# Optimization experiments

Hardware: AMD Instinct MI355X
Metric: run time of the kernel (lower is better)

## Reference

```python
import jax, jax.numpy as jnp
import numpy as np

B, N, D, H = 4, 2048, 512, 8
HD = D // H
SCALE = D ** (-0.5)  # module uses embed_dim**-0.5, not head_dim**-0.5


def setup_inputs() -> dict:
    key = jax.random.key(0)
    k1, k2, k3, k4 = jax.random.split(key, 4)
    x = jax.random.normal(k1, (B, N, D), dtype=jnp.float32)
    # qkv: Linear(D, 3D, bias=False); store as [D, 3D] (x @ W_qkv)
    w_qkv = jax.random.normal(k2, (D, 3 * D), dtype=jnp.float32) * (D ** -0.5)
    # out_proj: Linear(D, D) with bias
    w_out = jax.random.normal(k3, (D, D), dtype=jnp.float32) * (D ** -0.5)
    b_out = jax.random.normal(k4, (D,), dtype=jnp.float32) * 0.01
    return {"x": x, "w_qkv": w_qkv, "w_out": w_out, "b_out": b_out}


def reference(x, w_qkv, w_out, b_out):
    # qkv projection -> [B, N, 3, H, HD] -> split
    qkv = (x @ w_qkv).reshape(B, N, 3, H, HD)
    q = qkv[:, :, 0].transpose(0, 2, 1, 3)  # [B, H, N, HD]
    k = qkv[:, :, 1].transpose(0, 2, 1, 3)
    v = qkv[:, :, 2].transpose(0, 2, 1, 3)
    attn = jnp.einsum("bhqd,bhkd->bhqk", q, k) * SCALE  # [B, H, N, N]
    attn = jax.nn.softmax(attn, axis=-1)
    out = jnp.einsum("bhqk,bhkd->bhqd", attn, v)  # [B, H, N, HD]
    out = out.transpose(0, 2, 1, 3).reshape(B, N, D)
    return out @ w_out + b_out
```

## Files before the change

### kernel.cpp

```cpp
#include <hip/hip_runtime.h>

typedef __attribute__((ext_vector_type(4))) float f32x4;
typedef __attribute__((ext_vector_type(16))) float f32x16;
typedef __attribute__((ext_vector_type(8))) short short8;

#define DEV static __device__ __forceinline__

DEV unsigned short f2bf(float f) {
  union { float f; unsigned u; } x; x.f = f;
  unsigned r = x.u + 0x7fffu + ((x.u >> 16) & 1u);
  return (unsigned short)(r >> 16);
}

DEV float bf2f(unsigned short u) {
  union { unsigned u; float f; } x; x.u = ((unsigned)u) << 16;
  return x.f;
}

DEV f32x4 mfma16(short8 a, short8 b, f32x4 c) {
  return __builtin_amdgcn_mfma_f32_16x16x32_bf16(a, b, c, 0, 0, 0);
}

DEV f32x16 mfma32(short8 a, short8 b, f32x16 c) {
  return __builtin_amdgcn_mfma_f32_32x32x16_bf16(a, b, c, 0, 0, 0);
}

DEV void gload16(const void* g, void* l) {
  __builtin_amdgcn_global_load_lds(
      (const __attribute__((address_space(1))) void*)g,
      (__attribute__((address_space(3))) void*)l, 16, 0, 0);
}

DEV float exp2f_fast(float x) {
  float r;
  asm("v_exp_f32 %0, %1" : "=v"(r) : "v"(x));
  return r;
}

DEV unsigned cvtpk(float lo, float hi) {
  unsigned r;
  asm("v_cvt_pk_bf16_f32 %0, %1, %2" : "=v"(r) : "v"(lo), "v"(hi));
  return r;
}

DEV short8 mk8(unsigned w0, unsigned w1, unsigned w2, unsigned w3) {
  union { unsigned u[4]; short8 s; } x;
  x.u[0] = w0; x.u[1] = w1; x.u[2] = w2; x.u[3] = w3;
  return x.s;
}

__global__ __launch_bounds__(256) void k_convert(const float* __restrict__ in,
                                                 unsigned short* __restrict__ out) {
  size_t i = (size_t)blockIdx.x * 256 + threadIdx.x;
  const f32x4* p = (const f32x4*)(in + i * 8);
  f32x4 a = p[0], b = p[1];
  short8 r;
  r[0] = f2bf(a[0]); r[1] = f2bf(a[1]); r[2] = f2bf(a[2]); r[3] = f2bf(a[3]);
  r[4] = f2bf(b[0]); r[5] = f2bf(b[1]); r[6] = f2bf(b[2]); r[7] = f2bf(b[3]);
  *(short8*)(out + i * 8) = r;
}

__global__ __launch_bounds__(256) void k_transpose_f32_bf16(
    const float* __restrict__ in, unsigned short* __restrict__ out, int R, int C) {
  __shared__ unsigned short T[64 * 72];
  int r0 = blockIdx.y * 64, c0 = blockIdx.x * 64;
  int t = threadIdx.x;
  int rr = t >> 2, seg = t & 3;
  const float* p = in + (size_t)(r0 + rr) * C + c0 + seg * 16;
#pragma unroll
  for (int q = 0; q < 4; ++q) {
    f32x4 v = *(const f32x4*)(p + q * 4);
#pragma unroll
    for (int e = 0; e < 4; ++e) T[rr * 72 + seg * 16 + q * 4 + e] = f2bf(v[e]);
  }
  __syncthreads();
  short8 o0, o1;
#pragma unroll
  for (int e = 0; e < 8; ++e) o0[e] = (short)T[(seg * 16 + e) * 72 + rr];
#pragma unroll
  for (int e = 0; e < 8; ++e) o1[e] = (short)T[(seg * 16 + 8 + e) * 72 + rr];
  unsigned short* q2 = out + (size_t)(c0 + rr) * R + r0 + seg * 16;
  *(short8*)q2 = o0;
  *(short8*)(q2 + 8) = o1;
}

__global__ __launch_bounds__(256) void k_build_vt(const unsigned short* __restrict__ qkv,
                                                  unsigned short* __restrict__ vt) {
  __shared__ unsigned short T[64 * 72];
  int n0 = blockIdx.x * 64;
  int bh = blockIdx.y;
  int b = bh >> 3, h = bh & 7;
  int t = threadIdx.x;
  int rr = t >> 2, seg = t & 3;
  const unsigned short* p =
      qkv + (size_t)(b * 2048 + n0 + rr) * 1536 + 1024 + h * 64 + seg * 16;
  *(short8*)&T[rr * 72 + seg * 16] = *(const short8*)p;
  *(short8*)&T[rr * 72 + seg * 16 + 8] = *(const short8*)(p + 8);
  __syncthreads();
  short8 o0, o1;
#pragma unroll
  for (int e = 0; e < 8; ++e) o0[e] = (short)T[(seg * 16 + e) * 72 + rr];
#pragma unroll
  for (int e = 0; e < 8; ++e) o1[e] = (short)T[(seg * 16 + 8 + e) * 72 + rr];
  unsigned short* q2 = vt + (size_t)(bh * 64 + rr) * 2048 + n0 + seg * 16;
  *(short8*)q2 = o0;
  *(short8*)(q2 + 8) = o1;
}

template <bool F32OUT>
__global__ __launch_bounds__(256) void k_gemm_bt(
    const unsigned short* __restrict__ A, const unsigned short* __restrict__ Bt,
    void* __restrict__ Cp, const float* __restrict__ bias, int M, int N, int K) {
  __shared__ unsigned short Asm[128 * 64];
  __shared__ unsigned short Bsm[128 * 64];
  const int tid = threadIdx.x;
  const int lane = tid & 63, w = tid >> 6;
  const int wr = w >> 1, wc = w & 1;
  const int bm = blockIdx.y * 128, bn = blockIdx.x * 128;
  const int l15 = lane & 15, l4 = lane >> 4;
  f32x4 acc[4][4] = {};
  for (int k0 = 0; k0 < K; k0 += 64) {
    __syncthreads();
#pragma unroll
    for (int j = 0; j < 4; ++j) {
      int c = j * 256 + tid;
      gload16(A + (size_t)(bm + (c >> 3)) * K + k0 + ((c & 7) << 3),
              Asm + (size_t)(j * 256 + w * 64) * 8);
    }
#pragma unroll
    for (int j = 0; j < 4; ++j) {
      int c = j * 256 + tid;
      gload16(Bt + (size_t)(bn + (c >> 3)) * K + k0 + ((c & 7) << 3),
              Bsm + (size_t)(j * 256 + w * 64) * 8);
    }
    __syncthreads();
#pragma unroll
    for (int kc = 0; kc < 2; ++kc) {
      short8 av[4], bv[4];
#pragma unroll
      for (int i = 0; i < 4; ++i)
        av[i] = *(const short8*)&Asm[(wr * 64 + i * 16 + l15) * 64 + kc * 32 + l4 * 8];
#pragma unroll
      for (int j = 0; j < 4; ++j)
        bv[j] = *(const short8*)&Bsm[(wc * 64 + j * 16 + l15) * 64 + kc * 32 + l4 * 8];
#pragma unroll
      for (int i = 0; i < 4; ++i)
#pragma unroll
        for (int j = 0; j < 4; ++j)
          acc[i][j] = mfma16(av[i], bv[j], acc[i][j]);
    }
  }
#pragma unroll
  for (int i = 0; i < 4; ++i) {
#pragma unroll
    for (int j = 0; j < 4; ++j) {
      int col = bn + wc * 64 + j * 16 + l15;
      float bb = 0.f;
      if constexpr (F32OUT) bb = bias[col];
#pragma unroll
      for (int v = 0; v < 4; ++v) {
        int row = bm + wr * 64 + i * 16 + l4 * 4 + v;
        if constexpr (F32OUT) {
          ((float*)Cp)[(size_t)row * N + col] = acc[i][j][v] + bb;
        } else {
          ((unsigned short*)Cp)[(size_t)row * N + col] = f2bf(acc[i][j][v]);
        }
      }
    }
  }
}

__global__ __launch_bounds__(256, 2) void k_attn2(const unsigned short* __restrict__ qkv,
                                                  const unsigned short* __restrict__ vtg,
                                                  unsigned short* __restrict__ O) {
  __shared__ unsigned short Ksm[2][64 * 64];
  __shared__ unsigned short Vsm[2][64 * 64];
  __shared__ float sml[4][32];
  const int tid = threadIdx.x;
  const int lane = tid & 63, w = tid >> 6;
  const int l31 = lane & 31, hi = lane >> 5;
  const int bh = blockIdx.y, b = bh >> 3, h = bh & 7;
  const int q0 = blockIdx.x * 128 + w * 32;
  const float CL = 0.044194173824159216f * 1.4426950408889634f;

  short8 qf[4];
  {
    const unsigned short* qp = qkv + (size_t)(b * 2048 + q0 + l31) * 1536 + h * 64;
#pragma unroll
    for (int ks = 0; ks < 4; ++ks) {
      short8 raw = *(const short8*)(qp + ks * 16 + hi * 8);
      short8 f;
#pragma unroll
      for (int e = 0; e < 8; ++e)
        f[e] = (short)f2bf(bf2f((unsigned short)raw[e]) * CL);
      qf[ks] = f;
    }
  }

  const int sr = tid >> 3, seg = tid & 7;
  const unsigned short* kg = qkv + (size_t)b * 2048 * 1536 + 512 + h * 64 + seg * 8;
  const unsigned short* vg = vtg + (size_t)bh * 64 * 2048 + seg * 8;
  const int wr1 = sr + 32;
  const int so0 = sr * 64 + ((seg * 8) ^ ((sr & 7) << 3));
  const int so1 = wr1 * 64 + ((seg * 8) ^ ((wr1 & 7) << 3));

  {
    short8 a = *(const short8*)(kg + (size_t)sr * 1536);
    short8 c = *(const short8*)(kg + (size_t)wr1 * 1536);
    short8 d0 = *(const short8*)(vg + (size_t)sr * 2048);
    short8 d1 = *(const short8*)(vg + (size_t)wr1 * 2048);
    *(short8*)&Ksm[0][so0] = a;  *(short8*)&Ksm[0][so1] = c;
    *(short8*)&Vsm[0][so0] = d0; *(short8*)&Vsm[0][so1] = d1;
  }
  __syncthreads();

  f32x16 oacc0 = {}, oacc1 = {};
  float m_run = 0.f, l_run = 0.f;
  const int rsw = (l31 & 7) << 3;

  for (int t = 0; t < 32; ++t) {
    const int cur = t & 1;
    const unsigned short* kb = Ksm[cur];
    const unsigned short* vb = Vsm[cur];

    short8 pk0, pk1, pv0, pv1;
    if (t < 31) {
      int kv = (t + 1) * 64;
      pk0 = *(const short8*)(kg + (size_t)(kv + sr) * 1536);
      pk1 = *(const short8*)(kg + (size_t)(kv + wr1) * 1536);
      pv0 = *(const short8*)(vg + (size_t)sr * 2048 + kv);
      pv1 = *(const short8*)(vg + (size_t)wr1 * 2048 + kv);
    }

    f32x16 st[2] = {};
#pragma unroll
    for (int ks = 0; ks < 4; ++ks) {
      int col = ks * 16 + hi * 8;
      short8 kf0 = *(const short8*)&kb[l31 * 64 + (col ^ rsw)];
      short8 kf1 = *(const short8*)&kb[(32 + l31) * 64 + (col ^ rsw)];
      st[0] = mfma32(kf0, qf[ks], st[0]);
      st[1] = mfma32(kf1, qf[ks], st[1]);
    }

    float tm[8];
#pragma unroll
    for (int r = 0; r < 8; ++r)
      tm[r] = fmaxf(fmaxf(st[0][r], st[0][r + 8]), fmaxf(st[1][r], st[1][r + 8]));
    float pm = fmaxf(fmaxf(fmaxf(tm[0], tm[1]), fmaxf(tm[2], tm[3])),
                     fmaxf(fmaxf(tm[4], tm[5]), fmaxf(tm[6], tm[7])));
    pm = fmaxf(pm, __shfl_xor(pm, 32));

    if (!__all(pm <= m_run + 11.5f)) {
      float mn = fmaxf(m_run, pm);
      float al = exp2f_fast(m_run - mn);
      sml[w][l31] = al;
#pragma unroll
      for (int r = 0; r < 16; ++r) {
        float a = sml[w][(r & 3) + 8 * (r >> 2) + 4 * hi];
        oacc0[r] *= a;
        oacc1[r] *= a;
      }
      l_run *= al;
      m_run = mn;
    }

    float lsum = 0.f;
    short8 pa[4];
#pragma unroll
    for (int s = 0; s < 2; ++s) {
      float p[16];
      float la = 0.f, lb = 0.f;
#pragma unroll
      for (int r = 0; r < 8; ++r) { p[r] = exp2f_fast(st[s][r] - m_run); la += p[r]; }
#pragma unroll
      for (int r = 8; r < 16; ++r) { p[r] = exp2f_fast(st[s][r] - m_run); lb += p[r]; }
      lsum += la + lb;
#pragma unroll
      for (int g = 0; g < 2; ++g) {
        unsigned pkA0 = cvtpk(p[8 * g + 0], p[8 * g + 1]);
        unsigned pkA1 = cvtpk(p[8 * g + 2], p[8 * g + 3]);
        unsigned pkB0 = cvtpk(p[8 * g + 4], p[8 * g + 5]);
        unsigned pkB1 = cvtpk(p[8 * g + 6], p[8 * g + 7]);
        unsigned tA0 = __shfl_xor(pkA0, 32), tA1 = __shfl_xor(pkA1, 32);
        unsigned tB0 = __shfl_xor(pkB0, 32), tB1 = __shfl_xor(pkB1, 32);
        unsigned w0 = hi ? tB0 : pkA0;
        unsigned w1 = hi ? tB1 : pkA1;
        unsigned w2 = hi ? pkB0 : tA0;
        unsigned w3 = hi ? pkB1 : tA1;
        pa[2 * s + g] = mk8(w0, w1, w2, w3);
      }
    }
    lsum += __shfl_xor(lsum, 32);
    l_run += lsum;

#pragma unroll
    for (int ks = 0; ks < 4; ++ks) {
      int col = ks * 16 + hi * 8;
      short8 vf0 = *(const short8*)&vb[l31 * 64 + (col ^ rsw)];
      short8 vf1 = *(const short8*)&vb[(32 + l31) * 64 + (col ^ rsw)];
      oacc0 = mfma32(pa[ks], vf0, oacc0);
      oacc1 = mfma32(pa[ks], vf1, oacc1);
    }

    if (t < 31) {
      unsigned short* kn = Ksm[cur ^ 1];
      unsigned short* vn = Vsm[cur ^ 1];
      *(short8*)&kn[so0] = pk0; *(short8*)&kn[so1] = pk1;
      *(short8*)&vn[so0] = pv0; *(short8*)&vn[so1] = pv1;
    }
    __syncthreads();
  }

  sml[w][l31] = l_run;
#pragma unroll
  for (int r = 0; r < 16; ++r) {
    int qd = (r & 3) + 8 * (r >> 2) + 4 * hi;
    float linv = 1.0f / sml[w][qd];
    size_t row = (size_t)(b * 2048 + q0 + qd) * 512 + h * 64;
    O[row + l31] = f2bf(oacc0[r] * linv);
    O[row + 32 + l31] = f2bf(oacc1[r] * linv);
  }
}

extern "C" void kernel_launch(void* const* d_in, const int* in_sizes, int n_in,
                              void* d_out, int out_size, void* d_ws, size_t ws_size,
                              hipStream_t stream) {
  const float* x = (const float*)d_in[0];
  const float* w_qkv = (const float*)d_in[1];
  const float* w_out = (const float*)d_in[2];
  const float* b_out = (const float*)d_in[3];
  float* out = (float*)d_out;
  char* ws = (char*)d_ws;

  unsigned short* xb    = (unsigned short*)(ws + 0);
  unsigned short* wqkvT = (unsigned short*)(ws + 8388608);
  unsigned short* woutT = (unsigned short*)(ws + 9961472);
  unsigned short* qkvb  = (unsigned short*)(ws + 10485760);
  unsigned short* vtb   = (unsigned short*)(ws + 35651584);
  unsigned short* Ob    = (unsigned short*)(ws + 44040192);

  k_convert<<<2048, 256, 0, stream>>>(x, xb);
  k_transpose_f32_bf16<<<dim3(24, 8), 256, 0, stream>>>(w_qkv, wqkvT, 512, 1536);
  k_transpose_f32_bf16<<<dim3(8, 8), 256, 0, stream>>>(w_out, woutT, 512, 512);
  k_gemm_bt<false><<<dim3(12, 64), 256, 0, stream>>>(xb, wqkvT, (void*)qkvb, nullptr,
                                                     8192, 1536, 512);
  k_build_vt<<<dim3(32, 32), 256, 0, stream>>>(qkvb, vtb);
  k_attn2<<<dim3(16, 32), 256, 0, stream>>>(qkvb, vtb, Ob);
  k_gemm_bt<true><<<dim3(4, 64), 256, 0, stream>>>(Ob, woutT, (void*)out, b_out,
                                                   8192, 512, 512);
}
```

Before: 183.5 us.

## Software-pipeline QK^T one tile ahead with triple-buffered V in attention

The attention kernel now computes the QK^T scores for tile t+1 while doing softmax and PV on tile t. Global prefetch moves to two tiles ahead, with K double-buffered and V triple-buffered in LDS. MFMA sections are wrapped in s_setprio so they get issue priority. The per-row rescale and normalise broadcasts now use lane shuffles instead of a shared-memory array. The cost is more registers (an extra pair of score accumulators) and more LDS, which may hurt occupancy at two blocks per CU.

New measurement: 184.7 us. About the same (+0.7%).

```diff
diff --git a/kernel.cpp b/kernel.cpp
--- a/kernel.cpp
+++ b/kernel.cpp
@@ -170,12 +170,11 @@
   }
 }
 
-__global__ __launch_bounds__(256, 2) void k_attn2(const unsigned short* __restrict__ qkv,
+__global__ __launch_bounds__(256, 2) void k_attn3(const unsigned short* __restrict__ qkv,
                                                   const unsigned short* __restrict__ vtg,
                                                   unsigned short* __restrict__ O) {
-  __shared__ unsigned short Ksm[2][64 * 64];
-  __shared__ unsigned short Vsm[2][64 * 64];
-  __shared__ float sml[4][32];
+  __shared__ unsigned short Ks[2][4096];
+  __shared__ unsigned short Vs[3][4096];
   const int tid = threadIdx.x;
   const int lane = tid & 63, w = tid >> 6;
   const int l31 = lane & 31, hi = lane >> 5;
@@ -200,52 +199,81 @@
   const int sr = tid >> 3, seg = tid & 7;
   const unsigned short* kg = qkv + (size_t)b * 2048 * 1536 + 512 + h * 64 + seg * 8;
   const unsigned short* vg = vtg + (size_t)bh * 64 * 2048 + seg * 8;
-  const int wr1 = sr + 32;
   const int so0 = sr * 64 + ((seg * 8) ^ ((sr & 7) << 3));
-  const int so1 = wr1 * 64 + ((seg * 8) ^ ((wr1 & 7) << 3));
+  const int so1 = so0 + 32 * 64;
 
   {
-    short8 a = *(const short8*)(kg + (size_t)sr * 1536);
-    short8 c = *(const short8*)(kg + (size_t)wr1 * 1536);
-    short8 d0 = *(const short8*)(vg + (size_t)sr * 2048);
-    short8 d1 = *(const short8*)(vg + (size_t)wr1 * 2048);
-    *(short8*)&Ksm[0][so0] = a;  *(short8*)&Ksm[0][so1] = c;
-    *(short8*)&Vsm[0][so0] = d0; *(short8*)&Vsm[0][so1] = d1;
+    short8 k0a = *(const short8*)(kg + (size_t)sr * 1536);
+    short8 k0b = *(const short8*)(kg + (size_t)(sr + 32) * 1536);
+    short8 v0a = *(const short8*)(vg + (size_t)sr * 2048);
+    short8 v0b = *(const short8*)(vg + (size_t)(sr + 32) * 2048);
+    short8 k1a = *(const short8*)(kg + (size_t)(64 + sr) * 1536);
+    short8 k1b = *(const short8*)(kg + (size_t)(64 + sr + 32) * 1536);
+    short8 v1a = *(const short8*)(vg + (size_t)sr * 2048 + 64);
+    short8 v1b = *(const short8*)(vg + (size_t)(sr + 32) * 2048 + 64);
+    *(short8*)&Ks[0][so0] = k0a; *(short8*)&Ks[0][so1] = k0b;
+    *(short8*)&Vs[0][so0] = v0a; *(short8*)&Vs[0][so1] = v0b;
+    *(short8*)&Ks[1][so0] = k1a; *(short8*)&Ks[1][so1] = k1b;
+    *(short8*)&Vs[1][so0] = v1a; *(short8*)&Vs[1][so1] = v1b;
   }
   __syncthreads();
 
-  f32x16 oacc0 = {}, oacc1 = {};
-  float m_run = 0.f, l_run = 0.f;
   const int rsw = (l31 & 7) << 3;
 
-  for (int t = 0; t < 32; ++t) {
-    const int cur = t & 1;
-    const unsigned short* kb = Ksm[cur];
-    const unsigned short* vb = Vsm[cur];
-
-    short8 pk0, pk1, pv0, pv1;
-    if (t < 31) {
-      int kv = (t + 1) * 64;
-      pk0 = *(const short8*)(kg + (size_t)(kv + sr) * 1536);
-      pk1 = *(const short8*)(kg + (size_t)(kv + wr1) * 1536);
-      pv0 = *(const short8*)(vg + (size_t)sr * 2048 + kv);
-      pv1 = *(const short8*)(vg + (size_t)wr1 * 2048 + kv);
-    }
-
-    f32x16 st[2] = {};
+  f32x16 st0 = {}, st1 = {};
+  {
+    const unsigned short* kb = Ks[0];
+    __builtin_amdgcn_s_setprio(1);
 #pragma unroll
     for (int ks = 0; ks < 4; ++ks) {
       int col = ks * 16 + hi * 8;
       short8 kf0 = *(const short8*)&kb[l31 * 64 + (col ^ rsw)];
       short8 kf1 = *(const short8*)&kb[(32 + l31) * 64 + (col ^ rsw)];
-      st[0] = mfma32(kf0, qf[ks], st[0]);
-      st[1] = mfma32(kf1, qf[ks], st[1]);
+      st0 = mfma32(kf0, qf[ks], st0);
+      st1 = mfma32(kf1, qf[ks], st1);
+    }
+    __builtin_amdgcn_s_setprio(0);
+  }
+  __syncthreads();
+
+  unsigned short* kread = Ks[1];
+  unsigned short* kwrite = Ks[0];
+  unsigned short* vcur = Vs[0];
+  unsigned short* vnxt = Vs[1];
+  unsigned short* vstg = Vs[2];
+
+  f32x16 oacc0 = {}, oacc1 = {};
+  float m_run = 0.f, l_run = 0.f;
+
+  for (int t = 0; t < 32; ++t) {
+    short8 pk0, pk1, pv0, pv1;
+    const bool has2 = (t < 30);
+    if (has2) {
+      int kv = (t + 2) * 64;
+      pk0 = *(const short8*)(kg + (size_t)(kv + sr) * 1536);
+      pk1 = *(const short8*)(kg + (size_t)(kv + sr + 32) * 1536);
+      pv0 = *(const short8*)(vg + (size_t)sr * 2048 + kv);
+      pv1 = *(const short8*)(vg + (size_t)(sr + 32) * 2048 + kv);
+    }
+
+    f32x16 ns0 = {}, ns1 = {};
+    if (t < 31) {
+      __builtin_amdgcn_s_setprio(1);
+#pragma unroll
+      for (int ks = 0; ks < 4; ++ks) {
+        int col = ks * 16 + hi * 8;
+        short8 kf0 = *(const short8*)&kread[l31 * 64 + (col ^ rsw)];
+        short8 kf1 = *(const short8*)&kread[(32 + l31) * 64 + (col ^ rsw)];
+        ns0 = mfma32(kf0, qf[ks], ns0);
+        ns1 = mfma32(kf1, qf[ks], ns1);
+      }
+      __builtin_amdgcn_s_setprio(0);
     }
 
     float tm[8];
 #pragma unroll
     for (int r = 0; r < 8; ++r)
-      tm[r] = fmaxf(fmaxf(st[0][r], st[0][r + 8]), fmaxf(st[1][r], st[1][r + 8]));
+      tm[r] = fmaxf(fmaxf(st0[r], st0[r + 8]), fmaxf(st1[r], st1[r + 8]));
     float pm = fmaxf(fmaxf(fmaxf(tm[0], tm[1]), fmaxf(tm[2], tm[3])),
                      fmaxf(fmaxf(tm[4], tm[5]), fmaxf(tm[6], tm[7])));
     pm = fmaxf(pm, __shfl_xor(pm, 32));
@@ -253,10 +281,10 @@
     if (!__all(pm <= m_run + 11.5f)) {
       float mn = fmaxf(m_run, pm);
       float al = exp2f_fast(m_run - mn);
-      sml[w][l31] = al;
 #pragma unroll
       for (int r = 0; r < 16; ++r) {
-        float a = sml[w][(r & 3) + 8 * (r >> 2) + 4 * hi];
+        int qd = (r & 3) + 8 * (r >> 2) + 4 * hi;
+        float a = __shfl(al, qd);
         oacc0[r] *= a;
         oacc1[r] *= a;
       }
@@ -268,12 +296,13 @@
     short8 pa[4];
 #pragma unroll
     for (int s = 0; s < 2; ++s) {
+      const f32x16& stv = s ? st1 : st0;
       float p[16];
       float la = 0.f, lb = 0.f;
 #pragma unroll
-      for (int r = 0; r < 8; ++r) { p[r] = exp2f_fast(st[s][r] - m_run); la += p[r]; }
-#pragma unroll
-      for (int r = 8; r < 16; ++r) { p[r] = exp2f_fast(st[s][r] - m_run); lb += p[r]; }
+      for (int r = 0; r < 8; ++r) { p[r] = exp2f_fast(stv[r] - m_run); la += p[r]; }
+#pragma unroll
+      for (int r = 8; r < 16; ++r) { p[r] = exp2f_fast(stv[r] - m_run); lb += p[r]; }
       lsum += la + lb;
 #pragma unroll
       for (int g = 0; g < 2; ++g) {
@@ -293,29 +322,32 @@
     lsum += __shfl_xor(lsum, 32);
     l_run += lsum;
 
+    __builtin_amdgcn_s_setprio(1);
 #pragma unroll
     for (int ks = 0; ks < 4; ++ks) {
       int col = ks * 16 + hi * 8;
-      short8 vf0 = *(const short8*)&vb[l31 * 64 + (col ^ rsw)];
-      short8 vf1 = *(const short8*)&vb[(32 + l31) * 64 + (col ^ rsw)];
+      short8 vf0 = *(const short8*)&vcur[l31 * 64 + (col ^ rsw)];
+      short8 vf1 = *(const short8*)&vcur[(32 + l31) * 64 + (col ^ rsw)];
       oacc0 = mfma32(pa[ks], vf0, oacc0);
       oacc1 = mfma32(pa[ks], vf1, oacc1);
     }
-
-    if (t < 31) {
-      unsigned short* kn = Ksm[cur ^ 1];
-      unsigned short* vn = Vsm[cur ^ 1];
-      *(short8*)&kn[so0] = pk0; *(short8*)&kn[so1] = pk1;
-      *(short8*)&vn[so0] = pv0; *(short8*)&vn[so1] = pv1;
+    __builtin_amdgcn_s_setprio(0);
+
+    if (has2) {
+      *(short8*)&kwrite[so0] = pk0; *(short8*)&kwrite[so1] = pk1;
+      *(short8*)&vstg[so0] = pv0;   *(short8*)&vstg[so1] = pv1;
     }
     __syncthreads();
-  }
-
-  sml[w][l31] = l_run;
+
+    st0 = ns0; st1 = ns1;
+    { unsigned short* tp = kread; kread = kwrite; kwrite = tp; }
+    { unsigned short* tp = vcur; vcur = vnxt; vnxt = vstg; vstg = tp; }
+  }
+
 #pragma unroll
   for (int r = 0; r < 16; ++r) {
     int qd = (r & 3) + 8 * (r >> 2) + 4 * hi;
-    float linv = 1.0f / sml[w][qd];
+    float linv = 1.0f / __shfl(l_run, qd);
     size_t row = (size_t)(b * 2048 + q0 + qd) * 512 + h * 64;
     O[row + l31] = f2bf(oacc0[r] * linv);
     O[row + 32 + l31] = f2bf(oacc1[r] * linv);
@@ -345,7 +377,7 @@
   k_gemm_bt<false><<<dim3(12, 64), 256, 0, stream>>>(xb, wqkvT, (void*)qkvb, nullptr,
                                                      8192, 1536, 512);
   k_build_vt<<<dim3(32, 32), 256, 0, stream>>>(qkvb, vtb);
-  k_attn2<<<dim3(16, 32), 256, 0, stream>>>(qkvb, vtb, Ob);
+  k_attn3<<<dim3(16, 32), 256, 0, stream>>>(qkvb, vtb, Ob);
   k_gemm_bt<true><<<dim3(4, 64), 256, 0, stream>>>(Ob, woutT, (void*)out, b_out,
                                                    8192, 512, 512);
 }
```

## Split attention KV tiles across two wave halves with final softmax merge

Applied to the files above, without the earlier changes.

The attention kernel doubles the block to 512 threads. Each group of four waves takes half of every 64-key tile (32 keys), keeps its own running max and sum, and the two partial outputs are merged through shared memory at the end. The point is to halve per-wave register pressure and work per iteration, so more waves are resident to hide the exp and MFMA latency. It also replaces the LDS round trip for the rescale factors with lane shuffles and adds s_setprio around the MFMA sections. The cost is an extra end-of-kernel merge pass plus a barrier, and each key tile's softmax is split across two independent running states.

After: 182.0 us. About the same (-0.8%).

```diff
diff --git a/kernel.cpp b/kernel.cpp
--- a/kernel.cpp
+++ b/kernel.cpp
@@ -170,17 +170,20 @@
   }
 }
 
-__global__ __launch_bounds__(256, 2) void k_attn2(const unsigned short* __restrict__ qkv,
+__global__ __launch_bounds__(512, 4) void k_attn4(const unsigned short* __restrict__ qkv,
                                                   const unsigned short* __restrict__ vtg,
                                                   unsigned short* __restrict__ O) {
-  __shared__ unsigned short Ksm[2][64 * 64];
-  __shared__ unsigned short Vsm[2][64 * 64];
-  __shared__ float sml[4][32];
+  __shared__ unsigned short smem[16896];
+  unsigned short* Ks0 = smem;
+  unsigned short* Ks1 = smem + 4096;
+  unsigned short* Vs0 = smem + 8192;
+  unsigned short* Vs1 = smem + 12288;
   const int tid = threadIdx.x;
   const int lane = tid & 63, w = tid >> 6;
+  const int qg = w & 3, half = w >> 2;
   const int l31 = lane & 31, hi = lane >> 5;
   const int bh = blockIdx.y, b = bh >> 3, h = bh & 7;
-  const int q0 = blockIdx.x * 128 + w * 32;
+  const int q0 = blockIdx.x * 128 + qg * 32;
   const float CL = 0.044194173824159216f * 1.4426950408889634f;
 
   short8 qf[4];
@@ -200,52 +203,41 @@
   const int sr = tid >> 3, seg = tid & 7;
   const unsigned short* kg = qkv + (size_t)b * 2048 * 1536 + 512 + h * 64 + seg * 8;
   const unsigned short* vg = vtg + (size_t)bh * 64 * 2048 + seg * 8;
-  const int wr1 = sr + 32;
-  const int so0 = sr * 64 + ((seg * 8) ^ ((sr & 7) << 3));
-  const int so1 = wr1 * 64 + ((seg * 8) ^ ((wr1 & 7) << 3));
-
-  {
-    short8 a = *(const short8*)(kg + (size_t)sr * 1536);
-    short8 c = *(const short8*)(kg + (size_t)wr1 * 1536);
-    short8 d0 = *(const short8*)(vg + (size_t)sr * 2048);
-    short8 d1 = *(const short8*)(vg + (size_t)wr1 * 2048);
-    *(short8*)&Ksm[0][so0] = a;  *(short8*)&Ksm[0][so1] = c;
-    *(short8*)&Vsm[0][so0] = d0; *(short8*)&Vsm[0][so1] = d1;
-  }
+  const int so = sr * 64 + ((seg * 8) ^ ((sr & 7) << 3));
+
+  *(short8*)&Ks0[so] = *(const short8*)(kg + (size_t)sr * 1536);
+  *(short8*)&Vs0[so] = *(const short8*)(vg + (size_t)sr * 2048);
   __syncthreads();
+
+  const int rsw = (l31 & 7) << 3;
+  const int krow = (half * 32 + l31) * 64;
 
   f32x16 oacc0 = {}, oacc1 = {};
   float m_run = 0.f, l_run = 0.f;
-  const int rsw = (l31 & 7) << 3;
+  unsigned short* kcur = Ks0; unsigned short* knxt = Ks1;
+  unsigned short* vcur = Vs0; unsigned short* vnxt = Vs1;
 
   for (int t = 0; t < 32; ++t) {
-    const int cur = t & 1;
-    const unsigned short* kb = Ksm[cur];
-    const unsigned short* vb = Vsm[cur];
-
-    short8 pk0, pk1, pv0, pv1;
+    short8 pk, pv;
     if (t < 31) {
       int kv = (t + 1) * 64;
-      pk0 = *(const short8*)(kg + (size_t)(kv + sr) * 1536);
-      pk1 = *(const short8*)(kg + (size_t)(kv + wr1) * 1536);
-      pv0 = *(const short8*)(vg + (size_t)sr * 2048 + kv);
-      pv1 = *(const short8*)(vg + (size_t)wr1 * 2048 + kv);
-    }
-
-    f32x16 st[2] = {};
+      pk = *(const short8*)(kg + (size_t)(kv + sr) * 1536);
+      pv = *(const short8*)(vg + (size_t)sr * 2048 + kv);
+    }
+
+    f32x16 st = {};
+    __builtin_amdgcn_s_setprio(1);
 #pragma unroll
     for (int ks = 0; ks < 4; ++ks) {
       int col = ks * 16 + hi * 8;
-      short8 kf0 = *(const short8*)&kb[l31 * 64 + (col ^ rsw)];
-      short8 kf1 = *(const short8*)&kb[(32 + l31) * 64 + (col ^ rsw)];
-      st[0] = mfma32(kf0, qf[ks], st[0]);
-      st[1] = mfma32(kf1, qf[ks], st[1]);
-    }
+      short8 kf = *(const short8*)&kcur[krow + (col ^ rsw)];
+      st = mfma32(kf, qf[ks], st);
+    }
+    __builtin_amdgcn_s_setprio(0);
 
     float tm[8];
 #pragma unroll
-    for (int r = 0; r < 8; ++r)
-      tm[r] = fmaxf(fmaxf(st[0][r], st[0][r + 8]), fmaxf(st[1][r], st[1][r + 8]));
+    for (int r = 0; r < 8; ++r) tm[r] = fmaxf(st[r], st[r + 8]);
     float pm = fmaxf(fmaxf(fmaxf(tm[0], tm[1]), fmaxf(tm[2], tm[3])),
                      fmaxf(fmaxf(tm[4], tm[5]), fmaxf(tm[6], tm[7])));
     pm = fmaxf(pm, __shfl_xor(pm, 32));
@@ -253,10 +245,10 @@
     if (!__all(pm <= m_run + 11.5f)) {
       float mn = fmaxf(m_run, pm);
       float al = exp2f_fast(m_run - mn);
-      sml[w][l31] = al;
 #pragma unroll
       for (int r = 0; r < 16; ++r) {
-        float a = sml[w][(r & 3) + 8 * (r >> 2) + 4 * hi];
+        int qd = (r & 3) + 8 * (r >> 2) + 4 * hi;
+        float a = __shfl(al, qd);
         oacc0[r] *= a;
         oacc1[r] *= a;
       }
@@ -264,61 +256,86 @@
       m_run = mn;
     }
 
-    float lsum = 0.f;
-    short8 pa[4];
-#pragma unroll
-    for (int s = 0; s < 2; ++s) {
-      float p[16];
-      float la = 0.f, lb = 0.f;
-#pragma unroll
-      for (int r = 0; r < 8; ++r) { p[r] = exp2f_fast(st[s][r] - m_run); la += p[r]; }
-#pragma unroll
-      for (int r = 8; r < 16; ++r) { p[r] = exp2f_fast(st[s][r] - m_run); lb += p[r]; }
-      lsum += la + lb;
-#pragma unroll
-      for (int g = 0; g < 2; ++g) {
-        unsigned pkA0 = cvtpk(p[8 * g + 0], p[8 * g + 1]);
-        unsigned pkA1 = cvtpk(p[8 * g + 2], p[8 * g + 3]);
-        unsigned pkB0 = cvtpk(p[8 * g + 4], p[8 * g + 5]);
-        unsigned pkB1 = cvtpk(p[8 * g + 6], p[8 * g + 7]);
-        unsigned tA0 = __shfl_xor(pkA0, 32), tA1 = __shfl_xor(pkA1, 32);
-        unsigned tB0 = __shfl_xor(pkB0, 32), tB1 = __shfl_xor(pkB1, 32);
-        unsigned w0 = hi ? tB0 : pkA0;
-        unsigned w1 = hi ? tB1 : pkA1;
-        unsigned w2 = hi ? pkB0 : tA0;
-        unsigned w3 = hi ? pkB1 : tA1;
-        pa[2 * s + g] = mk8(w0, w1, w2, w3);
-      }
+    float p[16];
+    float la = 0.f, lb = 0.f;
+#pragma unroll
+    for (int r = 0; r < 8; ++r) { p[r] = exp2f_fast(st[r] - m_run); la += p[r]; }
+#pragma unroll
+    for (int r = 8; r < 16; ++r) { p[r] = exp2f_fast(st[r] - m_run); lb += p[r]; }
+    float lsum = la + lb;
+    short8 pa[2];
+#pragma unroll
+    for (int g = 0; g < 2; ++g) {
+      unsigned pkA0 = cvtpk(p[8 * g + 0], p[8 * g + 1]);
+      unsigned pkA1 = cvtpk(p[8 * g + 2], p[8 * g + 3]);
+      unsigned pkB0 = cvtpk(p[8 * g + 4], p[8 * g + 5]);
+      unsigned pkB1 = cvtpk(p[8 * g + 6], p[8 * g + 7]);
+      unsigned tA0 = __shfl_xor(pkA0, 32), tA1 = __shfl_xor(pkA1, 32);
+      unsigned tB0 = __shfl_xor(pkB0, 32), tB1 = __shfl_xor(pkB1, 32);
+      unsigned w0 = hi ? tB0 : pkA0;
+      unsigned w1 = hi ? tB1 : pkA1;
+      unsigned w2 = hi ? pkB0 : tA0;
+      unsigned w3 = hi ? pkB1 : tA1;
+      pa[g] = mk8(w0, w1, w2, w3);
     }
     lsum += __shfl_xor(lsum, 32);
     l_run += lsum;
 
-#pragma unroll
-    for (int ks = 0; ks < 4; ++ks) {
-      int col = ks * 16 + hi * 8;
-      short8 vf0 = *(const short8*)&vb[l31 * 64 + (col ^ rsw)];
-      short8 vf1 = *(const short8*)&vb[(32 + l31) * 64 + (col ^ rsw)];
+    __builtin_amdgcn_s_setprio(1);
+#pragma unroll
+    for (int ks = 0; ks < 2; ++ks) {
+      int col = (half * 2 + ks) * 16 + hi * 8;
+      short8 vf0 = *(const short8*)&vcur[l31 * 64 + (col ^ rsw)];
+      short8 vf1 = *(const short8*)&vcur[(32 + l31) * 64 + (col ^ rsw)];
       oacc0 = mfma32(pa[ks], vf0, oacc0);
       oacc1 = mfma32(pa[ks], vf1, oacc1);
     }
+    __builtin_amdgcn_s_setprio(0);
 
     if (t < 31) {
-      unsigned short* kn = Ksm[cur ^ 1];
-      unsigned short* vn = Vsm[cur ^ 1];
-      *(short8*)&kn[so0] = pk0; *(short8*)&kn[so1] = pk1;
-      *(short8*)&vn[so0] = pv0; *(short8*)&vn[so1] = pv1;
+      *(short8*)&knxt[so] = pk;
+      *(short8*)&vnxt[so] = pv;
     }
     __syncthreads();
-  }
-
-  sml[w][l31] = l_run;
-#pragma unroll
-  for (int r = 0; r < 16; ++r) {
-    int qd = (r & 3) + 8 * (r >> 2) + 4 * hi;
-    float linv = 1.0f / sml[w][qd];
-    size_t row = (size_t)(b * 2048 + q0 + qd) * 512 + h * 64;
-    O[row + l31] = f2bf(oacc0[r] * linv);
-    O[row + 32 + l31] = f2bf(oacc1[r] * linv);
+    { unsigned short* tp = kcur; kcur = knxt; knxt = tp; }
+    { unsigned short* tp = vcur; vcur = vnxt; vnxt = tp; }
+  }
+
+  float* Opart = (float*)smem;
+  float* mlbuf = (float*)(smem + 16384);
+  if (half == 1) {
+    float* op = Opart + qg * 2048;
+#pragma unroll
+    for (int r = 0; r < 16; ++r) {
+      int qd = (r & 3) + 8 * (r >> 2) + 4 * hi;
+      op[qd * 64 + l31] = oacc0[r];
+      op[qd * 64 + 32 + l31] = oacc1[r];
+    }
+    if (hi == 0) {
+      mlbuf[qg * 64 + l31] = m_run;
+      mlbuf[qg * 64 + 32 + l31] = l_run;
+    }
+  }
+  __syncthreads();
+  if (half == 0) {
+    float mb = mlbuf[qg * 64 + l31];
+    float lb2 = mlbuf[qg * 64 + 32 + l31];
+    float mmax = fmaxf(m_run, mb);
+    float sa = exp2f_fast(m_run - mmax);
+    float sb = exp2f_fast(mb - mmax);
+    float dI = 1.0f / (l_run * sa + lb2 * sb);
+    float fA = sa * dI, fB = sb * dI;
+    const float* op = Opart + qg * 2048;
+#pragma unroll
+    for (int r = 0; r < 16; ++r) {
+      int qd = (r & 3) + 8 * (r >> 2) + 4 * hi;
+      float fa = __shfl(fA, qd), fb = __shfl(fB, qd);
+      float o0 = oacc0[r] * fa + op[qd * 64 + l31] * fb;
+      float o1 = oacc1[r] * fa + op[qd * 64 + 32 + l31] * fb;
+      size_t row = (size_t)(b * 2048 + q0 + qd) * 512 + h * 64;
+      O[row + l31] = f2bf(o0);
+      O[row + 32 + l31] = f2bf(o1);
+    }
   }
 }
 
@@ -345,7 +362,7 @@
   k_gemm_bt<false><<<dim3(12, 64), 256, 0, stream>>>(xb, wqkvT, (void*)qkvb, nullptr,
                                                      8192, 1536, 512);
   k_build_vt<<<dim3(32, 32), 256, 0, stream>>>(qkvb, vtb);
-  k_attn2<<<dim3(16, 32), 256, 0, stream>>>(qkvb, vtb, Ob);
+  k_attn4<<<dim3(16, 32), 512, 0, stream>>>(qkvb, vtb, Ob);
   k_gemm_bt<true><<<dim3(4, 64), 256, 0, stream>>>(Ob, woutT, (void*)out, b_out,
                                                    8192, 512, 512);
 }
```
